# Performance work log

Measured on AMD Instinct MI355X. Metric: run time of the kernel, lower is better.

## Reference

```python
import jax, jax.numpy as jnp
import numpy as np

B, T, C = 2, 2048, 2048
H, KVH, D = 16, 4, 128       # n_head, num_kv_heads, head_size
G = H // KVH                  # kv groups
SCALE = D ** -0.5
THETA = 10000.0


def setup_inputs() -> dict:
    key = jax.random.key(0)
    ks = jax.random.split(key, 5)
    s = 0.02
    return {
        "x": jax.random.normal(ks[0], (B, T, C), dtype=jnp.float32),
        "Wq": jax.random.normal(ks[1], (C, C), dtype=jnp.float32) * s,
        "bq": jnp.zeros((C,), jnp.float32),
        "Wk": jax.random.normal(ks[2], (C, KVH * D), dtype=jnp.float32) * s,
        "bk": jnp.zeros((KVH * D,), jnp.float32),
        "Wv": jax.random.normal(ks[3], (C, KVH * D), dtype=jnp.float32) * s,
        "bv": jnp.zeros((KVH * D,), jnp.float32),
        "Wo": jax.random.normal(ks[4], (C, C), dtype=jnp.float32) * s,
        "bo": jnp.zeros((C,), jnp.float32),
    }


def _rope(x):
    # x: [B, h, T, D]; interleaved-pair RoPE (lucidrains rotary-embedding-torch style)
    half = D // 2
    inv_freq = 1.0 / (THETA ** (jnp.arange(0, D, 2, dtype=jnp.float32) / D))  # [half]
    t = jnp.arange(T, dtype=jnp.float32)
    ang = t[:, None] * inv_freq[None, :]                 # [T, half]
    cos = jnp.repeat(jnp.cos(ang), 2, axis=-1)           # [T, D]
    sin = jnp.repeat(jnp.sin(ang), 2, axis=-1)
    xp = x.reshape(*x.shape[:-1], half, 2)
    x_rot = jnp.stack([-xp[..., 1], xp[..., 0]], axis=-1).reshape(x.shape)
    return x * cos + x_rot * sin


def reference(x, Wq, bq, Wk, bk, Wv, bv, Wo, bo):
    # projections
    q = (x @ Wq + bq).reshape(B, T, H, D).transpose(0, 2, 1, 3)      # [B,H,T,D]
    k = (x @ Wk + bk).reshape(B, T, KVH, D).transpose(0, 2, 1, 3)    # [B,KVH,T,D]
    v = (x @ Wv + bv).reshape(B, T, KVH, D).transpose(0, 2, 1, 3)
    # RoPE pre-attention
    q = _rope(q)
    k = _rope(k)
    # GQA: group query heads against shared KV heads (no repeat materialization)
    qg = q.reshape(B, KVH, G, T, D)
    att = jnp.einsum("bhgtd,bhsd->bhgts", qg, k) * SCALE              # [B,KVH,G,T,T]
    causal = jnp.tril(jnp.ones((T, T), dtype=bool))
    att = jnp.where(causal, att, jnp.float32(-jnp.inf))
    att = jax.nn.softmax(att, axis=-1)
    y = jnp.einsum("bhgts,bhsd->bhgtd", att, v)                        # [B,KVH,G,T,D]
    y = y.reshape(B, H, T, D).transpose(0, 2, 1, 3).reshape(B, T, C)
    return y @ Wo + bo
```

## Files before the change

### kernel.cpp

```cpp
#include <hip/hip_runtime.h>
#include <hip/hip_bf16.h>

typedef __bf16 bf16;
typedef __attribute__((ext_vector_type(8))) __bf16 bf16x8;
typedef __attribute__((ext_vector_type(4))) float f32x4;

#define SCALE2 (0.08838834764831845f * 1.4426950408889634f)

__device__ inline void gload16(const bf16* g, bf16* l) {
  __builtin_amdgcn_global_load_lds((const __attribute__((address_space(1))) void*)g,
                                   (__attribute__((address_space(3))) void*)l, 16, 0, 0);
}

__global__ __launch_bounds__(256)
void prep_all_kernel(const float* __restrict__ x, bf16* __restrict__ xb,
                     const float* __restrict__ bq, const float* __restrict__ bk,
                     const float* __restrict__ bv, float* __restrict__ bqkv,
                     float* __restrict__ cost, float* __restrict__ sint,
                     const float* __restrict__ Wq, const float* __restrict__ Wk,
                     const float* __restrict__ Wv, const float* __restrict__ Wo,
                     bf16* __restrict__ wqkvT, bf16* __restrict__ woT) {
  __shared__ bf16 tile[64][72];
  int bid = blockIdx.x;
  if (bid < 4096) {
    int i = bid * 256 + threadIdx.x;
    const float* p = x + (size_t)i * 8;
    float4 a = *(const float4*)p, b = *(const float4*)(p + 4);
    union { uint4 u; bf16 h[8]; } un;
    un.h[0] = (bf16)a.x; un.h[1] = (bf16)a.y; un.h[2] = (bf16)a.z; un.h[3] = (bf16)a.w;
    un.h[4] = (bf16)b.x; un.h[5] = (bf16)b.y; un.h[6] = (bf16)b.z; un.h[7] = (bf16)b.w;
    *(uint4*)(xb + (size_t)i * 8) = un.u;
  } else if (bid < 4608) {
    int idx = (bid - 4096) * 256 + threadIdx.x;
    int t = idx >> 6, i = idx & 63;
    float inv = expf(-(float)i * (logf(10000.f) / 64.f));
    float ang = (float)t * inv;
    cost[idx] = cosf(ang);
    sint[idx] = sinf(ang);
    if (idx < 3072)
      bqkv[idx] = (idx < 2048) ? bq[idx] : (idx < 2560 ? bk[idx - 2048] : bv[idx - 2560]);
  } else {
    int b2 = bid - 4608;
    int by = b2 / 80, bx = b2 - by * 80;
    const float* in; bf16* out; int N, n0;
    const int K = 2048;
    if (bx < 32)      { in = Wq; out = wqkvT;                        N = 2048; n0 = bx * 64; }
    else if (bx < 40) { in = Wk; out = wqkvT + (size_t)2048 * 2048; N = 512;  n0 = (bx - 32) * 64; }
    else if (bx < 48) { in = Wv; out = wqkvT + (size_t)2560 * 2048; N = 512;  n0 = (bx - 40) * 64; }
    else              { in = Wo; out = woT;                          N = 2048; n0 = (bx - 48) * 64; }
    int k0 = by * 64;
    int t = threadIdx.x;
    int r8 = t >> 5, c2 = (t & 31) * 2;
#pragma unroll
    for (int it = 0; it < 8; it++) {
      int row = it * 8 + r8;
      float2 v = *(const float2*)(in + (size_t)(k0 + row) * N + n0 + c2);
      tile[row][c2] = (bf16)v.x;
      tile[row][c2 + 1] = (bf16)v.y;
    }
    __syncthreads();
    int r = t >> 3, c = (t & 7) * 8;
    int rot = t & 7;
#pragma unroll
    for (int it = 0; it < 2; it++) {
      int rr = it * 32 + r;
      union { uint4 u; bf16 h[8]; } un;
#pragma unroll
      for (int j = 0; j < 8; j++) {
        int jj = (j + rot) & 7;
        un.h[jj] = tile[c + jj][rr];
      }
      *(uint4*)(out + (size_t)(n0 + rr) * K + k0 + c) = un.u;
    }
  }
}

__global__ __launch_bounds__(256)
void ropev_kernel(bf16* __restrict__ qkv, const float* __restrict__ cost,
                  const float* __restrict__ sint, bf16* __restrict__ vT) {
  __shared__ bf16 tile[64][72];
  if (blockIdx.x < 5120) {
    int p = blockIdx.x * 256 + threadIdx.x;
    if (p >= 4096 * 320) return;
    int row = p / 320;
    int rc = p - row * 320;
    int e = rc * 8;
    int t = row & 2047;
    int i0 = (e & 127) >> 1;
    bf16* ptr = qkv + (size_t)row * 3072 + e;
    float4 cv = *(const float4*)(cost + t * 64 + i0);
    float4 sv = *(const float4*)(sint + t * 64 + i0);
    float c[4] = {cv.x, cv.y, cv.z, cv.w}, s[4] = {sv.x, sv.y, sv.z, sv.w};
    union { uint4 u; bf16 h[8]; } un;
    un.u = *(const uint4*)ptr;
#pragma unroll
    for (int j = 0; j < 4; j++) {
      float x0 = (float)un.h[2 * j], x1 = (float)un.h[2 * j + 1];
      un.h[2 * j]     = (bf16)(x0 * c[j] - x1 * s[j]);
      un.h[2 * j + 1] = (bf16)(x1 * c[j] + x0 * s[j]);
    }
    *(uint4*)ptr = un.u;
  } else {
    int bid = blockIdx.x - 5120;
    int z = bid & 7;
    int yy = (bid >> 3) & 1;
    int xx = bid >> 4;
    int b = z >> 2, kvh = z & 3;
    int d0 = yy * 64;
    int t0 = xx * 64;
    const bf16* in = qkv + (size_t)(b * 2048) * 3072 + 2560 + kvh * 128;
    int t = threadIdx.x;
    int r = t >> 3, c = (t & 7) * 8;
#pragma unroll
    for (int it = 0; it < 2; it++) {
      int rr = it * 32 + r;
      *(uint4*)&tile[rr][c] = *(const uint4*)(in + (size_t)(t0 + rr) * 3072 + d0 + c);
    }
    __syncthreads();
    int rot = t & 7;
#pragma unroll
    for (int it = 0; it < 2; it++) {
      int rr = it * 32 + r;
      union { uint4 u; bf16 h[8]; } un;
#pragma unroll
      for (int j = 0; j < 8; j++) {
        int jj = (j + rot) & 7;
        un.h[jj] = tile[c + jj][rr];
      }
      *(uint4*)(vT + (size_t)(z * 128 + d0 + rr) * 2048 + t0 + c) = un.u;
    }
  }
}

template <typename OutT>
__global__ __launch_bounds__(256)
void gemm_bias_kernel(const bf16* __restrict__ A, const bf16* __restrict__ Bt,
                      const float* __restrict__ bias, OutT* __restrict__ C,
                      int M, int N, int K, int lda, int ldc) {
  __shared__ bf16 As[2][128 * 32];
  __shared__ bf16 Bs[2][128 * 32];
  int tid = threadIdx.x;
  int wv = tid >> 6, l = tid & 63;
  int wr = wv >> 1, wc = wv & 1;
  int lr = l & 15, g = l >> 4;

  int bid = blockIdx.y * gridDim.x + blockIdx.x;
  int cpx = (gridDim.x * gridDim.y) >> 3;
  int swz = (bid & 7) * cpx + (bid >> 3);
  int m0 = (swz / gridDim.x) * 128, n0 = (swz % gridDim.x) * 128;

  auto stage = [&](int k0, int buf) {
#pragma unroll
    for (int i = 0; i < 2; i++) {
      int e = i * 256 + tid;
      int row = e >> 2, c = e & 3;
      int csrc = (c ^ ((row >> 1) & 3)) * 8;
      gload16(A + (size_t)(m0 + row) * lda + k0 + csrc, &As[buf][(size_t)e * 8]);
      gload16(Bt + (size_t)(n0 + row) * K + k0 + csrc, &Bs[buf][(size_t)e * 8]);
    }
  };

  f32x4 acc[4][4] = {};
  stage(0, 0);
  __syncthreads();
  int cur = 0;
  int cswz = (g ^ ((lr >> 1) & 3)) * 8;
  for (int k0 = 32; k0 <= K; k0 += 32) {
    if (k0 < K) stage(k0, cur ^ 1);
    bf16x8 a[4], b[4];
#pragma unroll
    for (int mi = 0; mi < 4; mi++)
      a[mi] = *(const bf16x8*)&As[cur][(size_t)(wr * 64 + mi * 16 + lr) * 32 + cswz];
#pragma unroll
    for (int nj = 0; nj < 4; nj++)
      b[nj] = *(const bf16x8*)&Bs[cur][(size_t)(wc * 64 + nj * 16 + lr) * 32 + cswz];
#pragma unroll
    for (int mi = 0; mi < 4; mi++)
#pragma unroll
      for (int nj = 0; nj < 4; nj++)
        acc[mi][nj] = __builtin_amdgcn_mfma_f32_16x16x32_bf16(a[mi], b[nj], acc[mi][nj], 0, 0, 0);
    __syncthreads();
    cur ^= 1;
  }
#pragma unroll
  for (int nj = 0; nj < 4; nj++) {
    int gc = n0 + wc * 64 + nj * 16 + lr;
    float bv = bias[gc];
#pragma unroll
    for (int mi = 0; mi < 4; mi++) {
      int gr = m0 + wr * 64 + mi * 16 + g * 4;
#pragma unroll
      for (int reg = 0; reg < 4; reg++)
        C[(size_t)(gr + reg) * ldc + gc] = (OutT)(acc[mi][nj][reg] + bv);
    }
  }
}

__global__ __launch_bounds__(512, 4)
void attn_kernel(const bf16* __restrict__ qkv, const bf16* __restrict__ vT,
                 bf16* __restrict__ ybuf) {
  __shared__ bf16 Ks[64 * 128];
  __shared__ bf16 Vts[2][128 * 64];
  __shared__ bf16 Ps[8][16][72];

  int pair = blockIdx.x;
  int bh = blockIdx.y;
  int b = bh >> 4, h = bh & 15;
  int kvh = h >> 2;
  int tid = threadIdx.x, w = tid >> 6, l = tid & 63;
  int lr = l & 15, g = l >> 4, lk = g * 8;
  int wl = w & 3, wg = w >> 2;
  int qt = wg ? pair : 31 - pair;
  int q0 = qt * 64;
  int nt = 32 - pair;

  const bf16* kbase = qkv + (size_t)(b * 2048) * 3072 + 2048 + kvh * 128;
  const bf16* vtb   = vT + (size_t)(b * 4 + kvh) * 128 * 2048;
  f32x4 zero4 = {0.f, 0.f, 0.f, 0.f};

  auto stageK = [&](int kv0) {
#pragma unroll
    for (int it = 0; it < 2; it++) {
      int cidx = it * 512 + tid;
      int row = cidx >> 4, c = cidx & 15, csrc = c ^ (row & 7);
      gload16(kbase + (size_t)(kv0 + row) * 3072 + csrc * 8, &Ks[(size_t)cidx * 8]);
    }
  };
  auto stageV = [&](int kv0, int buf) {
#pragma unroll
    for (int it = 0; it < 2; it++) {
      int cidx = it * 512 + tid;
      int row = cidx >> 3, c = cidx & 7, csrc = c ^ (row & 7);
      gload16(vtb + (size_t)row * 2048 + kv0 + csrc * 8, &Vts[buf][(size_t)cidx * 8]);
    }
  };

  const bf16* qbase = qkv + (size_t)(b * 2048 + q0 + wl * 16 + lr) * 3072 + h * 128;
  bf16x8 qf[4];
#pragma unroll
  for (int kk = 0; kk < 4; kk++) {
    bf16x8 v = *(const bf16x8*)(qbase + kk * 32 + lk);
#pragma unroll
    for (int j = 0; j < 8; j++) v[j] = (bf16)((float)v[j] * SCALE2);
    qf[kk] = v;
  }

  float m_r = -1e30f, l_r = 0.f;
  f32x4 o_acc[8];
#pragma unroll
  for (int f = 0; f < 8; f++) o_acc[f] = zero4;

  stageK(0);
  stageV(0, 0);
  __syncthreads();
  int cur = 0;

  for (int kvt = 0; kvt < nt; kvt++) {
    int kv0 = kvt * 64;
    bool act = (kvt <= qt);

    f32x4 sa[4];
#pragma unroll
    for (int nj = 0; nj < 4; nj++) sa[nj] = zero4;
    if (act) {
      __builtin_amdgcn_s_setprio(1);
#pragma unroll
      for (int kk = 0; kk < 4; kk++) {
        int cmem = (kk * 4 + g) ^ (lr & 7);
#pragma unroll
        for (int nj = 0; nj < 4; nj++) {
          bf16x8 kf = *(const bf16x8*)&Ks[(size_t)((nj * 16 + lr) * 16 + cmem) * 8];
          sa[nj] = __builtin_amdgcn_mfma_f32_16x16x32_bf16(kf, qf[kk], sa[nj], 0, 0, 0);
        }
      }
      __builtin_amdgcn_s_setprio(0);
    }
    __syncthreads();

    if (kvt + 1 < nt) {
      stageK(kv0 + 64);
      stageV(kv0 + 64, cur ^ 1);
    }

    if (act) {
      bool diag = (kvt == qt);
      int qpos = q0 + wl * 16 + lr;
      float p[4][4];
#pragma unroll
      for (int nj = 0; nj < 4; nj++)
#pragma unroll
        for (int rg = 0; rg < 4; rg++) {
          float s = sa[nj][rg];
          if (diag && (kv0 + nj * 16 + g * 4 + rg > qpos)) s = -1e30f;
          p[nj][rg] = s;
        }

      float a0 = fmaxf(fmaxf(p[0][0], p[0][1]), fmaxf(p[0][2], p[0][3]));
      float a1 = fmaxf(fmaxf(p[1][0], p[1][1]), fmaxf(p[1][2], p[1][3]));
      float a2 = fmaxf(fmaxf(p[2][0], p[2][1]), fmaxf(p[2][2], p[2][3]));
      float a3 = fmaxf(fmaxf(p[3][0], p[3][1]), fmaxf(p[3][2], p[3][3]));
      float mx = fmaxf(fmaxf(a0, a1), fmaxf(a2, a3));
      mx = fmaxf(mx, __shfl_xor(mx, 16));
      mx = fmaxf(mx, __shfl_xor(mx, 32));

      if (__any(mx > m_r + 8.0f)) {
        float mnew = fmaxf(m_r, mx);
        float sc = exp2f(m_r - mnew);
        l_r *= sc;
        m_r = mnew;
        float osc[4];
#pragma unroll
        for (int rg = 0; rg < 4; rg++) osc[rg] = __shfl(sc, g * 4 + rg);
#pragma unroll
        for (int f = 0; f < 8; f++)
#pragma unroll
          for (int rg = 0; rg < 4; rg++) o_acc[f][rg] *= osc[rg];
      }

#pragma unroll
      for (int nj = 0; nj < 4; nj++)
#pragma unroll
        for (int rg = 0; rg < 4; rg++) p[nj][rg] = exp2f(p[nj][rg] - m_r);
      float s0 = (p[0][0] + p[0][1]) + (p[0][2] + p[0][3]);
      float s1 = (p[1][0] + p[1][1]) + (p[1][2] + p[1][3]);
      float s2 = (p[2][0] + p[2][1]) + (p[2][2] + p[2][3]);
      float s3 = (p[3][0] + p[3][1]) + (p[3][2] + p[3][3]);
      float rs = (s0 + s1) + (s2 + s3);
      rs += __shfl_xor(rs, 16);
      rs += __shfl_xor(rs, 32);
      l_r += rs;

#pragma unroll
      for (int nj = 0; nj < 4; nj++) {
        union { uint2 u; bf16 hh[4]; } pw;
#pragma unroll
        for (int rg = 0; rg < 4; rg++) pw.hh[rg] = (bf16)p[nj][rg];
        *(uint2*)&Ps[w][lr][nj * 16 + g * 4] = pw.u;
      }
      asm volatile("s_waitcnt lgkmcnt(0)" ::: "memory");
      __builtin_amdgcn_sched_barrier(0);

      __builtin_amdgcn_s_setprio(1);
#pragma unroll
      for (int kk2 = 0; kk2 < 2; kk2++) {
        bf16x8 pf = *(const bf16x8*)&Ps[w][lr][kk2 * 32 + lk];
        int cmem = (kk2 * 4 + g) ^ (lr & 7);
#pragma unroll
        for (int f = 0; f < 8; f++) {
          bf16x8 vf = *(const bf16x8*)&Vts[cur][(size_t)((f * 16 + lr) * 8 + cmem) * 8];
          o_acc[f] = __builtin_amdgcn_mfma_f32_16x16x32_bf16(pf, vf, o_acc[f], 0, 0, 0);
        }
      }
      __builtin_amdgcn_s_setprio(0);
    }
    __syncthreads();
    cur ^= 1;
  }

  float linv[4];
#pragma unroll
  for (int rg = 0; rg < 4; rg++) linv[rg] = 1.0f / __shfl(l_r, g * 4 + rg);
  size_t orow = (size_t)(b * 2048 + q0 + wl * 16);
#pragma unroll
  for (int rg = 0; rg < 4; rg++) {
    int r = g * 4 + rg;
#pragma unroll
    for (int f = 0; f < 8; f++) {
      float ov = o_acc[f][rg] * linv[rg];
      ybuf[(orow + r) * 2048 + h * 128 + f * 16 + lr] = (bf16)ov;
    }
  }
}

extern "C" void kernel_launch(void* const* d_in, const int* in_sizes, int n_in,
                              void* d_out, int out_size, void* d_ws, size_t ws_size,
                              hipStream_t stream) {
  const float* x  = (const float*)d_in[0];
  const float* Wq = (const float*)d_in[1];
  const float* bq = (const float*)d_in[2];
  const float* Wk = (const float*)d_in[3];
  const float* bk = (const float*)d_in[4];
  const float* Wv = (const float*)d_in[5];
  const float* bv = (const float*)d_in[6];
  const float* Wo = (const float*)d_in[7];
  const float* bo = (const float*)d_in[8];
  float* out = (float*)d_out;

  char* w = (char*)d_ws;
  auto alloc = [&](size_t bytes) { char* p = w; w += (bytes + 255) & ~(size_t)255; return p; };
  bf16*  xb    = (bf16*)alloc((size_t)4096 * 2048 * 2);
  bf16*  wqkvT = (bf16*)alloc((size_t)3072 * 2048 * 2);
  bf16*  woT   = (bf16*)alloc((size_t)2048 * 2048 * 2);
  bf16*  qkv   = (bf16*)alloc((size_t)4096 * 3072 * 2);
  bf16*  vTg   = (bf16*)alloc((size_t)8 * 128 * 2048 * 2);
  float* bqkv  = (float*)alloc((size_t)3072 * 4);
  float* cost  = (float*)alloc((size_t)2048 * 64 * 4);
  float* sint  = (float*)alloc((size_t)2048 * 64 * 4);
  bf16*  ybuf  = xb;

  prep_all_kernel<<<7168, 256, 0, stream>>>(x, xb, bq, bk, bv, bqkv, cost, sint,
                                            Wq, Wk, Wv, Wo, wqkvT, woT);
  gemm_bias_kernel<bf16><<<dim3(24, 32), 256, 0, stream>>>(xb, wqkvT, bqkv, qkv, 4096, 3072, 2048, 2048, 3072);
  ropev_kernel<<<5632, 256, 0, stream>>>(qkv, cost, sint, vTg);
  attn_kernel<<<dim3(16, 32), 512, 0, stream>>>(qkv, vTg, ybuf);
  gemm_bias_kernel<float><<<dim3(16, 32), 256, 0, stream>>>(ybuf, woT, bo, out, 4096, 2048, 2048, 2048, 2048);
}
```

Before: 246.8 us.

## Fuse RoPE into QKV GEMM epilogue for K and attention Q load

Result: no change. 243.9 us (-1.2%).

```diff
diff --git a/kernel.cpp b/kernel.cpp
--- a/kernel.cpp
+++ b/kernel.cpp
@@ -76,66 +76,40 @@
 }
 
 __global__ __launch_bounds__(256)
-void ropev_kernel(bf16* __restrict__ qkv, const float* __restrict__ cost,
-                  const float* __restrict__ sint, bf16* __restrict__ vT) {
+void transpose_v_kernel(const bf16* __restrict__ qkv, bf16* __restrict__ vT) {
   __shared__ bf16 tile[64][72];
-  if (blockIdx.x < 5120) {
-    int p = blockIdx.x * 256 + threadIdx.x;
-    if (p >= 4096 * 320) return;
-    int row = p / 320;
-    int rc = p - row * 320;
-    int e = rc * 8;
-    int t = row & 2047;
-    int i0 = (e & 127) >> 1;
-    bf16* ptr = qkv + (size_t)row * 3072 + e;
-    float4 cv = *(const float4*)(cost + t * 64 + i0);
-    float4 sv = *(const float4*)(sint + t * 64 + i0);
-    float c[4] = {cv.x, cv.y, cv.z, cv.w}, s[4] = {sv.x, sv.y, sv.z, sv.w};
+  int z = blockIdx.z;
+  int b = z >> 2, kvh = z & 3;
+  int d0 = blockIdx.y * 64;
+  int t0 = blockIdx.x * 64;
+  const bf16* in = qkv + (size_t)(b * 2048) * 3072 + 2560 + kvh * 128;
+  int t = threadIdx.x;
+  int r = t >> 3, c = (t & 7) * 8;
+#pragma unroll
+  for (int it = 0; it < 2; it++) {
+    int rr = it * 32 + r;
+    *(uint4*)&tile[rr][c] = *(const uint4*)(in + (size_t)(t0 + rr) * 3072 + d0 + c);
+  }
+  __syncthreads();
+  int rot = t & 7;
+#pragma unroll
+  for (int it = 0; it < 2; it++) {
+    int rr = it * 32 + r;
     union { uint4 u; bf16 h[8]; } un;
-    un.u = *(const uint4*)ptr;
-#pragma unroll
-    for (int j = 0; j < 4; j++) {
-      float x0 = (float)un.h[2 * j], x1 = (float)un.h[2 * j + 1];
-      un.h[2 * j]     = (bf16)(x0 * c[j] - x1 * s[j]);
-      un.h[2 * j + 1] = (bf16)(x1 * c[j] + x0 * s[j]);
-    }
-    *(uint4*)ptr = un.u;
-  } else {
-    int bid = blockIdx.x - 5120;
-    int z = bid & 7;
-    int yy = (bid >> 3) & 1;
-    int xx = bid >> 4;
-    int b = z >> 2, kvh = z & 3;
-    int d0 = yy * 64;
-    int t0 = xx * 64;
-    const bf16* in = qkv + (size_t)(b * 2048) * 3072 + 2560 + kvh * 128;
-    int t = threadIdx.x;
-    int r = t >> 3, c = (t & 7) * 8;
-#pragma unroll
-    for (int it = 0; it < 2; it++) {
-      int rr = it * 32 + r;
-      *(uint4*)&tile[rr][c] = *(const uint4*)(in + (size_t)(t0 + rr) * 3072 + d0 + c);
-    }
-    __syncthreads();
-    int rot = t & 7;
-#pragma unroll
-    for (int it = 0; it < 2; it++) {
-      int rr = it * 32 + r;
-      union { uint4 u; bf16 h[8]; } un;
-#pragma unroll
-      for (int j = 0; j < 8; j++) {
-        int jj = (j + rot) & 7;
-        un.h[jj] = tile[c + jj][rr];
-      }
-      *(uint4*)(vT + (size_t)(z * 128 + d0 + rr) * 2048 + t0 + c) = un.u;
-    }
-  }
-}
-
-template <typename OutT>
+#pragma unroll
+    for (int j = 0; j < 8; j++) {
+      int jj = (j + rot) & 7;
+      un.h[jj] = tile[c + jj][rr];
+    }
+    *(uint4*)(vT + (size_t)(z * 128 + d0 + rr) * 2048 + t0 + c) = un.u;
+  }
+}
+
+template <typename OutT, bool ROPEK>
 __global__ __launch_bounds__(256)
 void gemm_bias_kernel(const bf16* __restrict__ A, const bf16* __restrict__ Bt,
                       const float* __restrict__ bias, OutT* __restrict__ C,
+                      const float* __restrict__ cost, const float* __restrict__ sint,
                       int M, int N, int K, int lda, int ldc) {
   __shared__ bf16 As[2][128 * 32];
   __shared__ bf16 Bs[2][128 * 32];
@@ -182,22 +156,35 @@
     __syncthreads();
     cur ^= 1;
   }
+  bool doRope = ROPEK && (n0 >= 2048) && (n0 < 2560);
 #pragma unroll
   for (int nj = 0; nj < 4; nj++) {
     int gc = n0 + wc * 64 + nj * 16 + lr;
     float bv = bias[gc];
+    int ti = (gc & 127) >> 1;
+    float sgn = (gc & 1) ? 1.f : -1.f;
 #pragma unroll
     for (int mi = 0; mi < 4; mi++) {
       int gr = m0 + wr * 64 + mi * 16 + g * 4;
 #pragma unroll
-      for (int reg = 0; reg < 4; reg++)
-        C[(size_t)(gr + reg) * ldc + gc] = (OutT)(acc[mi][nj][reg] + bv);
+      for (int reg = 0; reg < 4; reg++) {
+        float v = acc[mi][nj][reg] + bv;
+        if (doRope) {
+          float pv = __shfl_xor(v, 1);
+          int t = (gr + reg) & 2047;
+          float c = cost[t * 64 + ti];
+          float s = sint[t * 64 + ti];
+          v = v * c + sgn * pv * s;
+        }
+        C[(size_t)(gr + reg) * ldc + gc] = (OutT)v;
+      }
     }
   }
 }
 
 __global__ __launch_bounds__(512, 4)
 void attn_kernel(const bf16* __restrict__ qkv, const bf16* __restrict__ vT,
+                 const float* __restrict__ cost, const float* __restrict__ sint,
                  bf16* __restrict__ ybuf) {
   __shared__ bf16 Ks[64 * 128];
   __shared__ bf16 Vts[2][128 * 64];
@@ -235,13 +222,22 @@
     }
   };
 
-  const bf16* qbase = qkv + (size_t)(b * 2048 + q0 + wl * 16 + lr) * 3072 + h * 128;
+  int qrow = q0 + wl * 16 + lr;
+  const bf16* qbase = qkv + (size_t)(b * 2048 + qrow) * 3072 + h * 128;
   bf16x8 qf[4];
 #pragma unroll
   for (int kk = 0; kk < 4; kk++) {
     bf16x8 v = *(const bf16x8*)(qbase + kk * 32 + lk);
-#pragma unroll
-    for (int j = 0; j < 8; j++) v[j] = (bf16)((float)v[j] * SCALE2);
+    int i0 = kk * 16 + g * 4;
+    float4 cv = *(const float4*)(cost + qrow * 64 + i0);
+    float4 sv = *(const float4*)(sint + qrow * 64 + i0);
+    float cc[4] = {cv.x, cv.y, cv.z, cv.w}, ss[4] = {sv.x, sv.y, sv.z, sv.w};
+#pragma unroll
+    for (int j = 0; j < 4; j++) {
+      float x0 = (float)v[2 * j], x1 = (float)v[2 * j + 1];
+      v[2 * j]     = (bf16)((x0 * cc[j] - x1 * ss[j]) * SCALE2);
+      v[2 * j + 1] = (bf16)((x1 * cc[j] + x0 * ss[j]) * SCALE2);
+    }
     qf[kk] = v;
   }
 
@@ -400,8 +396,10 @@
 
   prep_all_kernel<<<7168, 256, 0, stream>>>(x, xb, bq, bk, bv, bqkv, cost, sint,
                                             Wq, Wk, Wv, Wo, wqkvT, woT);
-  gemm_bias_kernel<bf16><<<dim3(24, 32), 256, 0, stream>>>(xb, wqkvT, bqkv, qkv, 4096, 3072, 2048, 2048, 3072);
-  ropev_kernel<<<5632, 256, 0, stream>>>(qkv, cost, sint, vTg);
-  attn_kernel<<<dim3(16, 32), 512, 0, stream>>>(qkv, vTg, ybuf);
-  gemm_bias_kernel<float><<<dim3(16, 32), 256, 0, stream>>>(ybuf, woT, bo, out, 4096, 2048, 2048, 2048, 2048);
-}
+  gemm_bias_kernel<bf16, true><<<dim3(24, 32), 256, 0, stream>>>(
+      xb, wqkvT, bqkv, qkv, cost, sint, 4096, 3072, 2048, 2048, 3072);
+  transpose_v_kernel<<<dim3(32, 2, 8), 256, 0, stream>>>(qkv, vTg);
+  attn_kernel<<<dim3(16, 32), 512, 0, stream>>>(qkv, vTg, cost, sint, ybuf);
+  gemm_bias_kernel<float, false><<<dim3(16, 32), 256, 0, stream>>>(
+      ybuf, woT, bo, out, nullptr, nullptr, 4096, 2048, 2048, 2048, 2048);
+}
```
